# Optimization experiments

Hardware: AMD Instinct MI355X
Metric: run time of the kernel (lower is better)

The kernel has to match this reference:

```python
import jax, jax.numpy as jnp
import numpy as np

N_QUBITS = 15
DIM = 2 ** N_QUBITS  # 32768

# (op, arg1, arg2): ('R', theta_index, wire) or ('C', control, target)
GATES = [
    ('R', 0, 0), ('R', 1, 1), ('C', 0, 1),
    ('R', 2, 2), ('R', 3, 3), ('C', 3, 2),
    ('R', 4, 4), ('R', 5, 5), ('C', 4, 5),
    ('R', 6, 6), ('R', 7, 7), ('C', 7, 6),
    ('R', 8, 8), ('R', 9, 9), ('C', 8, 9),
    ('R', 10, 10), ('R', 11, 11), ('C', 11, 10),
    ('R', 12, 12), ('R', 13, 13), ('C', 8, 9),
    ('R', 14, 14),
    ('R', 15, 1), ('R', 16, 2), ('C', 1, 2),
    ('R', 14, 5), ('R', 15, 6), ('C', 6, 5),
    ('R', 16, 9), ('R', 17, 10), ('C', 9, 10),
    ('R', 18, 13), ('R', 19, 14), ('C', 9, 10),
    ('R', 19, 2), ('R', 20, 5), ('C', 2, 5),
    ('R', 21, 10), ('R', 22, 13), ('C', 13, 10),
    ('R', 23, 5), ('R', 24, 10),
    ('R', 25, 0), ('R', 26, 5), ('C', 0, 5),
    ('R', 27, 10), ('R', 28, 14), ('C', 14, 10),
    ('R', 29, 5), ('R', 30, 10),
]


def _ry(state, theta, w):
    """Batched RY on qubit w. state: [N, DIM] real (RY/CNOT keep it real).
    theta: scalar or [N]."""
    n = state.shape[0]
    s = state.reshape(n, 2 ** w, 2, 2 ** (N_QUBITS - 1 - w))
    half = theta * 0.5
    c = jnp.reshape(jnp.atleast_1d(jnp.cos(half)), (-1, 1, 1))
    sn = jnp.reshape(jnp.atleast_1d(jnp.sin(half)), (-1, 1, 1))
    a0 = s[:, :, 0, :]
    a1 = s[:, :, 1, :]
    out = jnp.stack([c * a0 - sn * a1, sn * a0 + c * a1], axis=2)
    return out.reshape(n, DIM)


def _cnot(state, control, target):
    n = state.shape[0]
    lo, hi = (control, target) if control < target else (target, control)
    s = state.reshape(n, 2 ** lo, 2, 2 ** (hi - lo - 1), 2, 2 ** (N_QUBITS - 1 - hi))
    cx, tx = (2, 4) if control == lo else (4, 2)
    c0 = jax.lax.index_in_dim(s, 0, cx, keepdims=True)
    c1 = jnp.flip(jax.lax.index_in_dim(s, 1, cx, keepdims=True), axis=tx)
    s = jnp.concatenate([c0, c1], axis=cx)
    return s.reshape(n, DIM)


def _expz(state, w):
    """<Z_w> = P(bit w = 0) - P(bit w = 1)."""
    n = state.shape[0]
    p = jnp.sum(state.reshape(n, 2 ** w, 2, -1) ** 2, axis=(1, 3))
    return p[:, 0] - p[:, 1]


def _circuit(M, theta):
    """M: [N, 15] per-node input angles; theta: [31] shared angles."""
    n = M.shape[0]
    state = jnp.zeros((n, DIM), dtype=M.dtype).at[:, 0].set(1.0)
    for w in range(N_QUBITS):
        state = _ry(state, M[:, w], w)
    for op, a, b in GATES:
        if op == 'R':
            state = _ry(state, theta[a], b)
        else:
            state = _cnot(state, a, b)
    z = jnp.stack([_expz(state, 5), _expz(state, 10)], axis=1)  # [N, 2]
    return jnp.pi * (1.0 - z)  # 2*pi*(1 - <Z>)/2


def setup_inputs() -> dict:
    key = jax.random.key(0)
    k1, k2, k3, k4, k5 = jax.random.split(key, 5)
    N, E = 128, 1024
    X = jax.random.normal(k1, (N, E // E * 5), dtype=jnp.float32)  # [N, 5]
    e = jax.random.uniform(k2, (E,), dtype=jnp.float32)
    # one-hot incidence matrices (each edge touches one input and one output node)
    Ri = jax.nn.one_hot(jax.random.randint(k3, (E,), 0, N), N, dtype=jnp.float32).T
    Ro = jax.nn.one_hot(jax.random.randint(k4, (E,), 0, N), N, dtype=jnp.float32).T
    theta = jax.random.uniform(k5, (31,), dtype=jnp.float32, maxval=2.0 * np.pi)
    return {"X": X, "e": e, "Ri": Ri, "Ro": Ro, "theta": theta}


def reference(X, e, Ri, Ro, theta):
    bo = Ro.T @ X            # [E, 5]
    bi = Ri.T @ X            # [E, 5]
    Rwi = Ri * e             # [N, E], e broadcasts over rows
    Rwo = Ro * e
    mi = Rwi @ bo            # [N, 5]
    mo = Rwo @ bi            # [N, 5]
    M = jnp.concatenate([mi, mo, X], axis=1)  # [N, 15]
    return _circuit(M, theta)  # [N, 2]
```

## Files before the change

### kernel.cpp

```cpp
#include <hip/hip_runtime.h>

namespace {
constexpr int NNODES = 128;
constexpr int NEDGES = 1024;
constexpr int CAP    = 96;
constexpr float PI_F = 3.14159265358979323846f;
}

__global__ __launch_bounds__(256)
void nodenet_fused(const float* __restrict__ X,
                   const float* __restrict__ ew,
                   const float* __restrict__ Ri,
                   const float* __restrict__ Ro,
                   const float* __restrict__ theta,
                   float* __restrict__ out)
{
    __shared__ float Xs[NNODES * 5];
    __shared__ float Mang[15];
    __shared__ int   cin, cout;
    __shared__ int   inE[CAP];  __shared__ float inW[CAP];
    __shared__ int   inO[CAP];  __shared__ float inV[CAP];
    __shared__ int   outE[CAP]; __shared__ float outW[CAP];
    __shared__ int   outR[CAP]; __shared__ float outV[CAP];

    const int n = blockIdx.x, tid = threadIdx.x;
    const int lane = tid & 63, wid = tid >> 6;

    for (int i = tid; i < NNODES * 5; i += 256) Xs[i] = X[i];
    if (tid < 10) Mang[tid] = 0.f;
    else if (tid < 15) Mang[tid] = X[n * 5 + (tid - 10)];
    if (tid == 0) { cin = 0; cout = 0; }
    __syncthreads();

    #pragma unroll
    for (int j = 0; j < 4; ++j) {
        const int e = tid + j * 256;
        const float riv = Ri[n * NEDGES + e];
        const float rov = Ro[n * NEDGES + e];
        if (riv != 0.f) {
            const int idx = atomicAdd(&cin, 1);
            if (idx < CAP) { inE[idx] = e; inW[idx] = riv * ew[e]; }
        }
        if (rov != 0.f) {
            const int idx = atomicAdd(&cout, 1);
            if (idx < CAP) { outE[idx] = e; outW[idx] = rov * ew[e]; }
        }
    }
    __syncthreads();

    const int ci = min(cin, CAP), co = min(cout, CAP);
    const int total = ci + co;
    for (int t = wid; t < total; t += 4) {
        const bool isIn = (t < ci);
        const int  e    = isIn ? inE[t] : outE[t - ci];
        const float* col = isIn ? Ro : Ri;
        const float v0 = col[lane * NEDGES + e];
        const float v1 = col[(lane + 64) * NEDGES + e];
        if (isIn) {
            if (lane == 0)  { inO[t] = 0; inV[t] = 0.f; }
            if (v0 != 0.f)  { inO[t] = lane;      inV[t] = v0; }
            if (v1 != 0.f)  { inO[t] = lane + 64; inV[t] = v1; }
        } else {
            const int j = t - ci;
            if (lane == 0)  { outR[j] = 0; outV[j] = 0.f; }
            if (v0 != 0.f)  { outR[j] = lane;      outV[j] = v0; }
            if (v1 != 0.f)  { outR[j] = lane + 64; outV[j] = v1; }
        }
    }
    __syncthreads();

    if (tid < ci) {
        const float wv = inW[tid] * inV[tid];
        const int   o  = inO[tid];
        #pragma unroll
        for (int k = 0; k < 5; ++k) atomicAdd(&Mang[k], wv * Xs[o * 5 + k]);
    } else if (tid >= 128 && tid - 128 < co) {
        const int   j  = tid - 128;
        const float wv = outW[j] * outV[j];
        const int   r  = outR[j];
        #pragma unroll
        for (int k = 0; k < 5; ++k) atomicAdd(&Mang[5 + k], wv * Xs[r * 5 + k]);
    }
    __syncthreads();
    if (wid >= 2) return;

    float c_, s_, t_, v0, v1, v2, v3;
#define CS(i)        __sincosf(0.5f * theta[i], &s_, &c_)

    if (wid == 0) {
        float ic[8], is[8];
        #pragma unroll
        for (int q = 0; q < 8; ++q) __sincosf(0.5f * Mang[q], &is[q], &ic[q]);

        float lp = 1.f;
        #pragma unroll
        for (int q = 2; q < 8; ++q) lp *= ((lane >> (q - 2)) & 1) ? is[q] : ic[q];
        float r0 = lp * ic[0] * ic[1];
        float r1 = lp * is[0] * ic[1];
        float r2 = lp * ic[0] * is[1];
        float r3 = lp * is[0] * is[1];

#define RY_REG0      { t_ = r0; r0 = c_*t_ - s_*r1; r1 = fmaf(s_, t_, c_*r1); \
                       t_ = r2; r2 = c_*t_ - s_*r3; r3 = fmaf(s_, t_, c_*r3); }
#define RY_REG1      { t_ = r0; r0 = c_*t_ - s_*r2; r2 = fmaf(s_, t_, c_*r2); \
                       t_ = r1; r1 = c_*t_ - s_*r3; r3 = fmaf(s_, t_, c_*r3); }
#define RY_LANE_A(sh){ const float sg = ((lane >> (sh)) & 1) ? s_ : -s_;      \
                       v0 = __shfl_xor(r0, 1 << (sh), 64);                    \
                       v1 = __shfl_xor(r1, 1 << (sh), 64);                    \
                       v2 = __shfl_xor(r2, 1 << (sh), 64);                    \
                       v3 = __shfl_xor(r3, 1 << (sh), 64);                    \
                       r0 = fmaf(c_, r0, sg*v0); r1 = fmaf(c_, r1, sg*v1);    \
                       r2 = fmaf(c_, r2, sg*v2); r3 = fmaf(c_, r3, sg*v3); }
#define CX_LL_A(csh, tsh) { const bool p = (lane >> (csh)) & 1;               \
                       v0 = __shfl_xor(r0, 1 << (tsh), 64);                   \
                       v1 = __shfl_xor(r1, 1 << (tsh), 64);                   \
                       v2 = __shfl_xor(r2, 1 << (tsh), 64);                   \
                       v3 = __shfl_xor(r3, 1 << (tsh), 64);                   \
                       if (p) { r0 = v0; r1 = v1; r2 = v2; r3 = v3; } }

        CS(0);  RY_REG0;
        CS(1);  RY_REG1;
        t_ = r1; r1 = r3; r3 = t_;
        CS(2);  RY_LANE_A(0);
        CS(3);  RY_LANE_A(1);
        CX_LL_A(1, 0);
        CS(4);  RY_LANE_A(2);
        CS(5);  RY_LANE_A(3);
        CX_LL_A(2, 3);
        CS(6);  RY_LANE_A(4);
        CS(7);  RY_LANE_A(5);
        CX_LL_A(5, 4);
        CS(15); RY_REG1;
        CS(16); RY_LANE_A(0);
        r2 = __shfl_xor(r2, 1, 64);
        r3 = __shfl_xor(r3, 1, 64);
        CS(14); RY_LANE_A(3);
        CS(15); RY_LANE_A(4);
        CX_LL_A(4, 3);
        CS(19); RY_LANE_A(0);
        CS(20); RY_LANE_A(3);
        CX_LL_A(0, 3);
        CS(23); RY_LANE_A(3);
        CS(25); RY_REG0;
        CS(26); RY_LANE_A(3);
        r1 = __shfl_xor(r1, 8, 64);
        r3 = __shfl_xor(r3, 8, 64);
        CS(29); RY_LANE_A(3);

        float zA = (r0*r0 + r1*r1 + r2*r2 + r3*r3) * (((lane >> 3) & 1) ? -1.f : 1.f);
        #pragma unroll
        for (int m = 1; m < 64; m <<= 1) zA += __shfl_xor(zA, m, 64);
        if (lane == 0) out[n * 2 + 0] = PI_F * (1.f - zA);
    } else {
        float c8, s8, c9, s9, c10, s10, c11, s11, c13, s13, c14, s14;
        __sincosf(0.5f * Mang[8],  &s8,  &c8);
        __sincosf(0.5f * Mang[9],  &s9,  &c9);
        __sincosf(0.5f * Mang[10], &s10, &c10);
        __sincosf(0.5f * Mang[11], &s11, &c11);
        __sincosf(0.5f * Mang[13], &s13, &c13);
        __sincosf(0.5f * Mang[14], &s14, &c14);

        float b = ((lane >> 0) & 1) ? s8  : c8;
        b      *= ((lane >> 1) & 1) ? s9  : c9;
        b      *= ((lane >> 2) & 1) ? s10 : c10;
        b      *= ((lane >> 3) & 1) ? s11 : c11;
        b      *= ((lane >> 4) & 1) ? s13 : c13;
        b      *= ((lane >> 5) & 1) ? s14 : c14;

#define RY_B(sh)     { const float sg = ((lane >> (sh)) & 1) ? s_ : -s_;      \
                       v0 = __shfl_xor(b, 1 << (sh), 64);                     \
                       b = fmaf(c_, b, sg*v0); }
#define CX_B(csh, tsh) { v0 = __shfl_xor(b, 1 << (tsh), 64);                  \
                       if ((lane >> (csh)) & 1) b = v0; }

        CS(8);  RY_B(0);
        CS(9);  RY_B(1);
        CX_B(0, 1);
        CS(10); RY_B(2);
        CS(11); RY_B(3);
        CX_B(3, 2);
        CS(13); RY_B(4);
        CX_B(0, 1);
        CS(14); RY_B(5);
        CS(16); RY_B(1);
        CS(17); RY_B(2);
        CX_B(1, 2);
        CS(18); RY_B(4);
        CS(19); RY_B(5);
        CX_B(1, 2);
        CS(21); RY_B(2);
        CS(22); RY_B(4);
        CX_B(4, 2);
        CS(24); RY_B(2);
        CS(27); RY_B(2);
        CS(28); RY_B(5);
        CX_B(5, 2);
        CS(30); RY_B(2);

        float zB = (b * b) * (((lane >> 2) & 1) ? -1.f : 1.f);
        #pragma unroll
        for (int m = 1; m < 64; m <<= 1) zB += __shfl_xor(zB, m, 64);
        if (lane == 0) out[n * 2 + 1] = PI_F * (1.f - zB);
    }
#undef CS
#undef RY_REG0
#undef RY_REG1
#undef RY_LANE_A
#undef CX_LL_A
#undef RY_B
#undef CX_B
}

extern "C" void kernel_launch(void* const* d_in, const int* in_sizes, int n_in,
                              void* d_out, int out_size, void* d_ws, size_t ws_size,
                              hipStream_t stream) {
    (void)in_sizes; (void)n_in; (void)d_ws; (void)ws_size; (void)out_size;
    const float* X     = (const float*)d_in[0];
    const float* ew    = (const float*)d_in[1];
    const float* Ri    = (const float*)d_in[2];
    const float* Ro    = (const float*)d_in[3];
    const float* theta = (const float*)d_in[4];
    float* out = (float*)d_out;

    nodenet_fused<<<NNODES, 256, 0, stream>>>(X, ew, Ri, Ro, theta, out);
}
```

Before: 12.88 us.

## Replace shared-memory atomic aggregation with per-wave shuffle reductions and batched gathers

Removes the shared X staging, the Mang shared array and the atomicAdd reduction phase along with one block barrier. Each of the two surviving waves now computes the angle sums it needs directly from global X and reduces them with xor shuffles. The incidence-column gathers are unrolled into up to 12 independent loads per thread before any are consumed, so more memory latency can overlap. The cost is redundant global X reads per wave and extra registers. Relying on an unconditional write to clear entries is dropped, so slots with no nonzero entry are left uninitialised.

```diff
diff --git a/kernel.cpp b/kernel.cpp
--- a/kernel.cpp
+++ b/kernel.cpp
@@ -4,6 +4,7 @@
 constexpr int NNODES = 128;
 constexpr int NEDGES = 1024;
 constexpr int CAP    = 96;
+constexpr int NIT    = 12;
 constexpr float PI_F = 3.14159265358979323846f;
 }
 
@@ -15,8 +16,6 @@
                    const float* __restrict__ theta,
                    float* __restrict__ out)
 {
-    __shared__ float Xs[NNODES * 5];
-    __shared__ float Mang[15];
     __shared__ int   cin, cout;
     __shared__ int   inE[CAP];  __shared__ float inW[CAP];
     __shared__ int   inO[CAP];  __shared__ float inV[CAP];
@@ -26,9 +25,6 @@
     const int n = blockIdx.x, tid = threadIdx.x;
     const int lane = tid & 63, wid = tid >> 6;
 
-    for (int i = tid; i < NNODES * 5; i += 256) Xs[i] = X[i];
-    if (tid < 10) Mang[tid] = 0.f;
-    else if (tid < 15) Mang[tid] = X[n * 5 + (tid - 10)];
     if (tid == 0) { cin = 0; cout = 0; }
     __syncthreads();
 
@@ -50,36 +46,44 @@
 
     const int ci = min(cin, CAP), co = min(cout, CAP);
     const int total = ci + co;
-    for (int t = wid; t < total; t += 4) {
-        const bool isIn = (t < ci);
-        const int  e    = isIn ? inE[t] : outE[t - ci];
+
+    float va[NIT], vb[NIT];
+    #pragma unroll
+    for (int it = 0; it < NIT; ++it) {
+        const int t = wid + it * 4;
+        int e = 0;
+        const float* col = Ri;
+        if (t < ci)         { e = inE[t];       col = Ro; }
+        else if (t < total) { e = outE[t - ci]; col = Ri; }
+        va[it] = col[lane * NEDGES + e];
+        vb[it] = col[(lane + 64) * NEDGES + e];
+    }
+    #pragma unroll
+    for (int it = 0; it < NIT; ++it) {
+        const int t = wid + it * 4;
+        if (t < ci) {
+            if (va[it] != 0.f) { inO[t] = lane;      inV[t] = va[it]; }
+            if (vb[it] != 0.f) { inO[t] = lane + 64; inV[t] = vb[it]; }
+        } else if (t < total) {
+            const int s = t - ci;
+            if (va[it] != 0.f) { outR[s] = lane;      outV[s] = va[it]; }
+            if (vb[it] != 0.f) { outR[s] = lane + 64; outV[s] = vb[it]; }
+        }
+    }
+    for (int t = wid + NIT * 4; t < total; t += 4) {
+        const bool isIn = t < ci;
+        const int e = isIn ? inE[t] : outE[t - ci];
         const float* col = isIn ? Ro : Ri;
-        const float v0 = col[lane * NEDGES + e];
-        const float v1 = col[(lane + 64) * NEDGES + e];
+        const float v0f = col[lane * NEDGES + e];
+        const float v1f = col[(lane + 64) * NEDGES + e];
         if (isIn) {
-            if (lane == 0)  { inO[t] = 0; inV[t] = 0.f; }
-            if (v0 != 0.f)  { inO[t] = lane;      inV[t] = v0; }
-            if (v1 != 0.f)  { inO[t] = lane + 64; inV[t] = v1; }
+            if (v0f != 0.f) { inO[t] = lane;      inV[t] = v0f; }
+            if (v1f != 0.f) { inO[t] = lane + 64; inV[t] = v1f; }
         } else {
-            const int j = t - ci;
-            if (lane == 0)  { outR[j] = 0; outV[j] = 0.f; }
-            if (v0 != 0.f)  { outR[j] = lane;      outV[j] = v0; }
-            if (v1 != 0.f)  { outR[j] = lane + 64; outV[j] = v1; }
-        }
-    }
-    __syncthreads();
-
-    if (tid < ci) {
-        const float wv = inW[tid] * inV[tid];
-        const int   o  = inO[tid];
-        #pragma unroll
-        for (int k = 0; k < 5; ++k) atomicAdd(&Mang[k], wv * Xs[o * 5 + k]);
-    } else if (tid >= 128 && tid - 128 < co) {
-        const int   j  = tid - 128;
-        const float wv = outW[j] * outV[j];
-        const int   r  = outR[j];
-        #pragma unroll
-        for (int k = 0; k < 5; ++k) atomicAdd(&Mang[5 + k], wv * Xs[r * 5 + k]);
+            const int s = t - ci;
+            if (v0f != 0.f) { outR[s] = lane;      outV[s] = v0f; }
+            if (v1f != 0.f) { outR[s] = lane + 64; outV[s] = v1f; }
+        }
     }
     __syncthreads();
     if (wid >= 2) return;
@@ -88,9 +92,40 @@
 #define CS(i)        __sincosf(0.5f * theta[i], &s_, &c_)
 
     if (wid == 0) {
+        float v[8] = {0.f,0.f,0.f,0.f,0.f,0.f,0.f,0.f};
+        if (lane < ci) {
+            const float wv = inW[lane] * inV[lane];
+            const int o = inO[lane] * 5;
+            #pragma unroll
+            for (int k = 0; k < 5; ++k) v[k] = wv * X[o + k];
+        }
+        if (lane + 64 < ci) {
+            const float wv = inW[lane + 64] * inV[lane + 64];
+            const int o = inO[lane + 64] * 5;
+            #pragma unroll
+            for (int k = 0; k < 5; ++k) v[k] += wv * X[o + k];
+        }
+        if (lane < co) {
+            const float wv = outW[lane] * outV[lane];
+            const int r = outR[lane] * 5;
+            #pragma unroll
+            for (int k = 0; k < 3; ++k) v[5 + k] = wv * X[r + k];
+        }
+        if (lane + 64 < co) {
+            const float wv = outW[lane + 64] * outV[lane + 64];
+            const int r = outR[lane + 64] * 5;
+            #pragma unroll
+            for (int k = 0; k < 3; ++k) v[5 + k] += wv * X[r + k];
+        }
+        #pragma unroll
+        for (int m = 1; m < 64; m <<= 1) {
+            #pragma unroll
+            for (int k = 0; k < 8; ++k) v[k] += __shfl_xor(v[k], m, 64);
+        }
+
         float ic[8], is[8];
         #pragma unroll
-        for (int q = 0; q < 8; ++q) __sincosf(0.5f * Mang[q], &is[q], &ic[q]);
+        for (int q = 0; q < 8; ++q) __sincosf(0.5f * v[q], &is[q], &ic[q]);
 
         float lp = 1.f;
         #pragma unroll
@@ -152,13 +187,32 @@
         for (int m = 1; m < 64; m <<= 1) zA += __shfl_xor(zA, m, 64);
         if (lane == 0) out[n * 2 + 0] = PI_F * (1.f - zA);
     } else {
+        float va0 = 0.f, va1 = 0.f;
+        if (lane < co) {
+            const float wv = outW[lane] * outV[lane];
+            const int r = outR[lane] * 5;
+            va0 = wv * X[r + 3];
+            va1 = wv * X[r + 4];
+        }
+        if (lane + 64 < co) {
+            const float wv = outW[lane + 64] * outV[lane + 64];
+            const int r = outR[lane + 64] * 5;
+            va0 += wv * X[r + 3];
+            va1 += wv * X[r + 4];
+        }
+        #pragma unroll
+        for (int m = 1; m < 64; m <<= 1) {
+            va0 += __shfl_xor(va0, m, 64);
+            va1 += __shfl_xor(va1, m, 64);
+        }
+
         float c8, s8, c9, s9, c10, s10, c11, s11, c13, s13, c14, s14;
-        __sincosf(0.5f * Mang[8],  &s8,  &c8);
-        __sincosf(0.5f * Mang[9],  &s9,  &c9);
-        __sincosf(0.5f * Mang[10], &s10, &c10);
-        __sincosf(0.5f * Mang[11], &s11, &c11);
-        __sincosf(0.5f * Mang[13], &s13, &c13);
-        __sincosf(0.5f * Mang[14], &s14, &c14);
+        __sincosf(0.5f * va0,          &s8,  &c8);
+        __sincosf(0.5f * va1,          &s9,  &c9);
+        __sincosf(0.5f * X[n*5 + 0],   &s10, &c10);
+        __sincosf(0.5f * X[n*5 + 1],   &s11, &c11);
+        __sincosf(0.5f * X[n*5 + 3],   &s13, &c13);
+        __sincosf(0.5f * X[n*5 + 4],   &s14, &c14);
 
         float b = ((lane >> 0) & 1) ? s8  : c8;
         b      *= ((lane >> 1) & 1) ? s9  : c9;
```

Result: slower. 13.57 us (+5.4%).

## Split edge extraction into a prepass kernel and scan compact edge lists per node

Applied to the files above, without the earlier changes.

A new first kernel makes one coalesced pass over Ri and Ro and records, for each edge, its single receiver and sender node index and value in workspace. The per-node circuit kernel then scans these compact per-edge arrays, accumulates the message angles in registers, and reduces them with wave shuffles plus a small shared array. This replaces the old strided column gathers through Ri/Ro, the shared-memory atomic compaction, and the atomic accumulation. In exchange it adds a second kernel launch and a global round trip, and it relies on every column holding exactly one nonzero, since entries are otherwise left unwritten.

```diff
diff --git a/kernel.cpp b/kernel.cpp
--- a/kernel.cpp
+++ b/kernel.cpp
@@ -3,83 +3,67 @@
 namespace {
 constexpr int NNODES = 128;
 constexpr int NEDGES = 1024;
-constexpr int CAP    = 96;
 constexpr float PI_F = 3.14159265358979323846f;
 }
 
 __global__ __launch_bounds__(256)
-void nodenet_fused(const float* __restrict__ X,
-                   const float* __restrict__ ew,
-                   const float* __restrict__ Ri,
-                   const float* __restrict__ Ro,
-                   const float* __restrict__ theta,
-                   float* __restrict__ out)
+void edge_extract(const float* __restrict__ Ri,
+                  const float* __restrict__ Ro,
+                  int*   __restrict__ eR,  float* __restrict__ eRV,
+                  int*   __restrict__ eS,  float* __restrict__ eSV)
 {
-    __shared__ float Xs[NNODES * 5];
-    __shared__ float Mang[15];
-    __shared__ int   cin, cout;
-    __shared__ int   inE[CAP];  __shared__ float inW[CAP];
-    __shared__ int   inO[CAP];  __shared__ float inV[CAP];
-    __shared__ int   outE[CAP]; __shared__ float outW[CAP];
-    __shared__ int   outR[CAP]; __shared__ float outV[CAP];
-
+    const int e  = blockIdx.x * 256 + threadIdx.x;
+    const int m0 = blockIdx.y * 16;
+    float ri[16], ro[16];
+    #pragma unroll
+    for (int j = 0; j < 16; ++j) {
+        ri[j] = Ri[(m0 + j) * NEDGES + e];
+        ro[j] = Ro[(m0 + j) * NEDGES + e];
+    }
+    #pragma unroll
+    for (int j = 0; j < 16; ++j) {
+        if (ri[j] != 0.f) { eR[e] = m0 + j; eRV[e] = ri[j]; }
+        if (ro[j] != 0.f) { eS[e] = m0 + j; eSV[e] = ro[j]; }
+    }
+}
+
+__global__ __launch_bounds__(256)
+void node_circuit(const float* __restrict__ X,
+                  const float* __restrict__ ew,
+                  const int*   __restrict__ eR,  const float* __restrict__ eRV,
+                  const int*   __restrict__ eS,  const float* __restrict__ eSV,
+                  const float* __restrict__ theta,
+                  float* __restrict__ out)
+{
+    __shared__ float sang[4][10];
     const int n = blockIdx.x, tid = threadIdx.x;
     const int lane = tid & 63, wid = tid >> 6;
 
-    for (int i = tid; i < NNODES * 5; i += 256) Xs[i] = X[i];
-    if (tid < 10) Mang[tid] = 0.f;
-    else if (tid < 15) Mang[tid] = X[n * 5 + (tid - 10)];
-    if (tid == 0) { cin = 0; cout = 0; }
-    __syncthreads();
-
+    float acc[10];
+    #pragma unroll
+    for (int k = 0; k < 10; ++k) acc[k] = 0.f;
     #pragma unroll
     for (int j = 0; j < 4; ++j) {
         const int e = tid + j * 256;
-        const float riv = Ri[n * NEDGES + e];
-        const float rov = Ro[n * NEDGES + e];
-        if (riv != 0.f) {
-            const int idx = atomicAdd(&cin, 1);
-            if (idx < CAP) { inE[idx] = e; inW[idx] = riv * ew[e]; }
+        const int r = eR[e], s = eS[e];
+        const float p = eRV[e] * ew[e] * eSV[e];
+        if (r == n) {
+            #pragma unroll
+            for (int k = 0; k < 5; ++k) acc[k] = fmaf(p, X[s * 5 + k], acc[k]);
         }
-        if (rov != 0.f) {
-            const int idx = atomicAdd(&cout, 1);
-            if (idx < CAP) { outE[idx] = e; outW[idx] = rov * ew[e]; }
+        if (s == n) {
+            #pragma unroll
+            for (int k = 0; k < 5; ++k) acc[5 + k] = fmaf(p, X[r * 5 + k], acc[5 + k]);
         }
     }
-    __syncthreads();
-
-    const int ci = min(cin, CAP), co = min(cout, CAP);
-    const int total = ci + co;
-    for (int t = wid; t < total; t += 4) {
-        const bool isIn = (t < ci);
-        const int  e    = isIn ? inE[t] : outE[t - ci];
-        const float* col = isIn ? Ro : Ri;
-        const float v0 = col[lane * NEDGES + e];
-        const float v1 = col[(lane + 64) * NEDGES + e];
-        if (isIn) {
-            if (lane == 0)  { inO[t] = 0; inV[t] = 0.f; }
-            if (v0 != 0.f)  { inO[t] = lane;      inV[t] = v0; }
-            if (v1 != 0.f)  { inO[t] = lane + 64; inV[t] = v1; }
-        } else {
-            const int j = t - ci;
-            if (lane == 0)  { outR[j] = 0; outV[j] = 0.f; }
-            if (v0 != 0.f)  { outR[j] = lane;      outV[j] = v0; }
-            if (v1 != 0.f)  { outR[j] = lane + 64; outV[j] = v1; }
-        }
-    }
-    __syncthreads();
-
-    if (tid < ci) {
-        const float wv = inW[tid] * inV[tid];
-        const int   o  = inO[tid];
-        #pragma unroll
-        for (int k = 0; k < 5; ++k) atomicAdd(&Mang[k], wv * Xs[o * 5 + k]);
-    } else if (tid >= 128 && tid - 128 < co) {
-        const int   j  = tid - 128;
-        const float wv = outW[j] * outV[j];
-        const int   r  = outR[j];
-        #pragma unroll
-        for (int k = 0; k < 5; ++k) atomicAdd(&Mang[5 + k], wv * Xs[r * 5 + k]);
+    #pragma unroll
+    for (int m = 1; m < 64; m <<= 1) {
+        #pragma unroll
+        for (int k = 0; k < 10; ++k) acc[k] += __shfl_xor(acc[k], m, 64);
+    }
+    if (lane == 0) {
+        #pragma unroll
+        for (int k = 0; k < 10; ++k) sang[wid][k] = acc[k];
     }
     __syncthreads();
     if (wid >= 2) return;
@@ -88,9 +72,14 @@
 #define CS(i)        __sincosf(0.5f * theta[i], &s_, &c_)
 
     if (wid == 0) {
+        float v[8];
+        #pragma unroll
+        for (int k = 0; k < 8; ++k)
+            v[k] = sang[0][k] + sang[1][k] + sang[2][k] + sang[3][k];
+
         float ic[8], is[8];
         #pragma unroll
-        for (int q = 0; q < 8; ++q) __sincosf(0.5f * Mang[q], &is[q], &ic[q]);
+        for (int q = 0; q < 8; ++q) __sincosf(0.5f * v[q], &is[q], &ic[q]);
 
         float lp = 1.f;
         #pragma unroll
@@ -152,13 +141,16 @@
         for (int m = 1; m < 64; m <<= 1) zA += __shfl_xor(zA, m, 64);
         if (lane == 0) out[n * 2 + 0] = PI_F * (1.f - zA);
     } else {
+        const float m8 = sang[0][8] + sang[1][8] + sang[2][8] + sang[3][8];
+        const float m9 = sang[0][9] + sang[1][9] + sang[2][9] + sang[3][9];
+
         float c8, s8, c9, s9, c10, s10, c11, s11, c13, s13, c14, s14;
-        __sincosf(0.5f * Mang[8],  &s8,  &c8);
-        __sincosf(0.5f * Mang[9],  &s9,  &c9);
-        __sincosf(0.5f * Mang[10], &s10, &c10);
-        __sincosf(0.5f * Mang[11], &s11, &c11);
-        __sincosf(0.5f * Mang[13], &s13, &c13);
-        __sincosf(0.5f * Mang[14], &s14, &c14);
+        __sincosf(0.5f * m8,         &s8,  &c8);
+        __sincosf(0.5f * m9,         &s9,  &c9);
+        __sincosf(0.5f * X[n*5 + 0], &s10, &c10);
+        __sincosf(0.5f * X[n*5 + 1], &s11, &c11);
+        __sincosf(0.5f * X[n*5 + 3], &s13, &c13);
+        __sincosf(0.5f * X[n*5 + 4], &s14, &c14);
 
         float b = ((lane >> 0) & 1) ? s8  : c8;
         b      *= ((lane >> 1) & 1) ? s9  : c9;
@@ -214,7 +206,7 @@
 extern "C" void kernel_launch(void* const* d_in, const int* in_sizes, int n_in,
                               void* d_out, int out_size, void* d_ws, size_t ws_size,
                               hipStream_t stream) {
-    (void)in_sizes; (void)n_in; (void)d_ws; (void)ws_size; (void)out_size;
+    (void)in_sizes; (void)n_in; (void)ws_size; (void)out_size;
     const float* X     = (const float*)d_in[0];
     const float* ew    = (const float*)d_in[1];
     const float* Ri    = (const float*)d_in[2];
@@ -222,5 +214,12 @@
     const float* theta = (const float*)d_in[4];
     float* out = (float*)d_out;
 
-    nodenet_fused<<<NNODES, 256, 0, stream>>>(X, ew, Ri, Ro, theta, out);
-}
+    char* ws = (char*)d_ws;
+    int*   eR  = (int*)  (ws);
+    float* eRV = (float*)(ws + 4096);
+    int*   eS  = (int*)  (ws + 8192);
+    float* eSV = (float*)(ws + 12288);
+
+    edge_extract<<<dim3(4, 8), 256, 0, stream>>>(Ri, Ro, eR, eRV, eS, eSV);
+    node_circuit<<<NNODES, 256, 0, stream>>>(X, ew, eR, eRV, eS, eSV, theta, out);
+}
```

New measurement: 15.26 us. 18.6% more time.
